# Optimization experiments

Measured on AMD Instinct MI355X. Metric: run time of the kernel, lower is better.

The kernel has to match this reference:

```python
import jax, jax.numpy as jnp
import numpy as np

D_MODEL = 1024
N_HEADS = 16
D_HEAD = D_MODEL // N_HEADS
FF = 4 * D_MODEL
B, S = 1, 2048
ROPE_BASE = 10000.0
LN_EPS = 1e-5


def setup_inputs() -> dict:
    key = jax.random.key(0)
    ks = jax.random.split(key, 12)
    sd = 0.02
    return {
        "x": jax.random.normal(ks[0], (B, S, D_MODEL), dtype=jnp.float32),
        # weights stored [in, out]
        "w_qkv": jax.random.normal(ks[1], (D_MODEL, 3 * D_MODEL), dtype=jnp.float32) * sd,
        "w_attn": jax.random.normal(ks[2], (D_MODEL, D_MODEL), dtype=jnp.float32) * sd,
        "b_attn": jnp.zeros((D_MODEL,), dtype=jnp.float32),
        "w_ff1": jax.random.normal(ks[3], (D_MODEL, FF), dtype=jnp.float32) * sd,
        "b_ff1": jnp.zeros((FF,), dtype=jnp.float32),
        "w_ff2": jax.random.normal(ks[4], (FF, D_MODEL), dtype=jnp.float32) * sd,
        "b_ff2": jnp.zeros((D_MODEL,), dtype=jnp.float32),
        "ln1_g": jnp.ones((D_MODEL,), dtype=jnp.float32),
        "ln1_b": jnp.zeros((D_MODEL,), dtype=jnp.float32),
        "ln2_g": jnp.ones((D_MODEL,), dtype=jnp.float32),
        "ln2_b": jnp.zeros((D_MODEL,), dtype=jnp.float32),
    }


def _layernorm(x, g, b):
    mu = jnp.mean(x, axis=-1, keepdims=True)
    var = jnp.mean(jnp.square(x - mu), axis=-1, keepdims=True)
    return (x - mu) * jax.lax.rsqrt(var + LN_EPS) * g + b


def _rope_cos_sin(seq_len, d_head, dtype):
    # scale=1.0 -> dynamic YaRN degenerates to vanilla RoPE with mscale=1
    inv_freq = 1.0 / (ROPE_BASE ** (jnp.arange(0, d_head, 2, dtype=jnp.float32) / d_head))
    pos = jnp.arange(seq_len, dtype=jnp.float32)
    freqs = pos[:, None] * inv_freq[None, :]          # [S, D/2]
    emb = jnp.concatenate([freqs, freqs], axis=-1)    # [S, D]
    return jnp.cos(emb).astype(dtype), jnp.sin(emb).astype(dtype)


def _rotate_half(x):
    x1, x2 = jnp.split(x, 2, axis=-1)
    return jnp.concatenate([-x2, x1], axis=-1)


def _apply_rope(q, k, cos, sin):
    # q,k: [B,S,H,D]; cos/sin: [S,D]
    c = cos[None, :, None, :]
    s = sin[None, :, None, :]
    return q * c + _rotate_half(q) * s, k * c + _rotate_half(k) * s


def _block(x, w_qkv, w_attn, b_attn, w_ff1, b_ff1, w_ff2, b_ff2,
           ln1_g, ln1_b, ln2_g, ln2_b):
    b, s, d = x.shape
    # --- attention sub-block (pre-norm) ---
    h = _layernorm(x, ln1_g, ln1_b)
    qkv = h @ w_qkv                                   # [B,S,3D]
    xq, xk, xv = jnp.split(qkv, 3, axis=-1)
    xq = xq.reshape(b, s, N_HEADS, D_HEAD)
    xk = xk.reshape(b, s, N_HEADS, D_HEAD)
    xv = xv.reshape(b, s, N_HEADS, D_HEAD)
    cos, sin = _rope_cos_sin(s, D_HEAD, x.dtype)
    xq, xk = _apply_rope(xq, xk, cos, sin)
    scale = 1.0 / np.sqrt(D_HEAD)
    scores = jnp.einsum("bqhd,bkhd->bhqk", xq, xk) * scale
    causal = jnp.tril(jnp.ones((s, s), dtype=bool))
    scores = jnp.where(causal[None, None], scores, jnp.finfo(scores.dtype).min)
    probs = jax.nn.softmax(scores, axis=-1)
    att = jnp.einsum("bhqk,bkhd->bqhd", probs, xv).reshape(b, s, d)
    x = x + (att @ w_attn + b_attn)
    # --- feed-forward sub-block (pre-norm) ---
    h2 = _layernorm(x, ln2_g, ln2_b)
    ff = jax.nn.gelu(h2 @ w_ff1 + b_ff1, approximate=False) @ w_ff2 + b_ff2
    return x + ff


def reference(x, w_qkv, w_attn, b_attn, w_ff1, b_ff1, w_ff2, b_ff2,
              ln1_g, ln1_b, ln2_g, ln2_b):
    return _block(x, w_qkv, w_attn, b_attn, w_ff1, b_ff1, w_ff2, b_ff2,
                  ln1_g, ln1_b, ln2_g, ln2_b)
```

## Files before the change

### kernel.cpp

```cpp
#include <hip/hip_runtime.h>
#include <hip/hip_bf16.h>
#include <stdint.h>

#define DM   1024
#define SEQ  2048
#define NH   16
#define DH   64
#define FFD  4096

typedef float  f32x4  __attribute__((ext_vector_type(4)));
typedef __bf16 bf16x8 __attribute__((ext_vector_type(8)));
typedef unsigned short u16;
typedef unsigned short u16x8 __attribute__((ext_vector_type(8)));

__device__ __forceinline__ u16 f2bf(float f){
    unsigned int u = __builtin_bit_cast(unsigned int, f);
    u = u + 0x7FFFu + ((u >> 16) & 1u);
    return (u16)(u >> 16);
}
__device__ __forceinline__ float bf2f(u16 v){
    unsigned int u = ((unsigned int)v) << 16;
    return __builtin_bit_cast(float, u);
}
__device__ __forceinline__ f32x4 zero4(){ f32x4 v; v[0]=0.f;v[1]=0.f;v[2]=0.f;v[3]=0.f; return v; }

__device__ __forceinline__ void gload_lds16(const void* g, void* l){
    __builtin_amdgcn_global_load_lds(
        (const __attribute__((address_space(1))) unsigned int*)(uintptr_t)g,
        (__attribute__((address_space(3))) unsigned int*)(uintptr_t)l,
        16, 0, 0);
}

__global__ __launch_bounds__(256) void transall_k(const float* __restrict__ s0, u16* __restrict__ d0,
                                                  const float* __restrict__ s1, u16* __restrict__ d1,
                                                  const float* __restrict__ s2, u16* __restrict__ d2,
                                                  const float* __restrict__ s3, u16* __restrict__ d3){
    __shared__ float tile[64][65];
    const int b = blockIdx.x;
    const float* src; u16* dst; int K, N, bx, by;
    if (b < 768)      { src = s0; dst = d0; K = 1024; N = 3072; bx = b % 48;          by = b / 48; }
    else if (b < 1024){ src = s1; dst = d1; K = 1024; N = 1024; bx = (b-768) % 16;    by = (b-768) / 16; }
    else if (b < 2048){ src = s2; dst = d2; K = 1024; N = 4096; bx = (b-1024) % 64;   by = (b-1024) / 64; }
    else              { src = s3; dst = d3; K = 4096; N = 1024; bx = (b-2048) % 16;   by = (b-2048) / 16; }
    const int n0 = bx * 64, k0 = by * 64;
    const int t = threadIdx.x;
#pragma unroll
    for (int i = 0; i < 16; ++i){
        int idx = t + i * 256;
        int r = idx >> 6, c = idx & 63;
        tile[r][c] = src[(size_t)(k0 + r) * N + n0 + c];
    }
    __syncthreads();
#pragma unroll
    for (int i = 0; i < 16; ++i){
        int idx = t + i * 256;
        int r = idx >> 6, c = idx & 63;
        dst[(size_t)(n0 + r) * K + k0 + c] = f2bf(tile[c][r]);
    }
}

__global__ __launch_bounds__(256) void ln_k(const float* __restrict__ in,
                                            const float* __restrict__ gw,
                                            const float* __restrict__ bw,
                                            u16* __restrict__ out){
    const int row = blockIdx.x, t = threadIdx.x;
    f32x4 vv = *((const f32x4*)(in + (size_t)row * DM) + t);
    float v[4];
#pragma unroll
    for (int j = 0; j < 4; ++j) v[j] = vv[j];
    float s = 0.f, ss = 0.f;
#pragma unroll
    for (int j = 0; j < 4; ++j){ s += v[j]; ss += v[j] * v[j]; }
#pragma unroll
    for (int off = 1; off < 64; off <<= 1){
        s  += __shfl_xor(s,  off, 64);
        ss += __shfl_xor(ss, off, 64);
    }
    __shared__ float rs_[4], rss_[4];
    const int w = t >> 6;
    if ((t & 63) == 0){ rs_[w] = s; rss_[w] = ss; }
    __syncthreads();
    s  = rs_[0] + rs_[1] + rs_[2] + rs_[3];
    ss = rss_[0] + rss_[1] + rss_[2] + rss_[3];
    const float mean = s * (1.f / DM);
    const float var  = ss * (1.f / DM) - mean * mean;
    const float rstd = rsqrtf(var + 1e-5f);
#pragma unroll
    for (int j = 0; j < 4; ++j){
        int c = t * 4 + j;
        out[(size_t)row * DM + c] = f2bf((v[j] - mean) * rstd * gw[c] + bw[c]);
    }
}

template<int TM, int TN, int WR, int WC, int EPI>
__global__ __launch_bounds__(256) void gemm_k(const u16* __restrict__ A,
                                              const u16* __restrict__ Bt,
                                              const float* __restrict__ bias,
                                              const float* __restrict__ resid,
                                              void* __restrict__ out,
                                              u16* __restrict__ qout,
                                              u16* __restrict__ kout,
                                              u16* __restrict__ vout,
                                              int M, int N, int K){
    constexpr int MR   = TM / WR / 16;
    constexpr int NR   = TN / WC / 16;
    constexpr int AISS = (TM * 64) / 4096;
    constexpr int BISS = (TN * 64) / 4096;
    __shared__ u16 ldsAll[2 * TM * 32 + 2 * TN * 32];
    u16* ldsA = ldsAll;
    u16* ldsB = ldsAll + 2 * TM * 32;
    const int t = threadIdx.x;
    const int L = t & 63, w = t >> 6;
    const int g = L >> 4, li = L & 15;
    const int wr = w / WC, wc = w % WC;
    const int rowbase = wr * (TM / WR);
    const int colbase = wc * (TN / WC);
    const int brow = blockIdx.x * TM, bcol = blockIdx.y * TN;

    const u16* aPtr = A  + (size_t)brow * K;
    const u16* bPtr = Bt + (size_t)bcol * K;

    f32x4 acc[MR][NR];
#pragma unroll
    for (int m = 0; m < MR; ++m)
#pragma unroll
        for (int n = 0; n < NR; ++n) acc[m][n] = zero4();

    auto STAGE = [&](int buf, int ko){
#pragma unroll
        for (int i = 0; i < AISS; ++i){
            int o = i * 256 + t;
            gload_lds16(aPtr + (size_t)(o >> 2) * K + (o & 3) * 8 + ko, &ldsA[buf * TM * 32 + o * 8]);
        }
#pragma unroll
        for (int i = 0; i < BISS; ++i){
            int o = i * 256 + t;
            gload_lds16(bPtr + (size_t)(o >> 2) * K + (o & 3) * 8 + ko, &ldsB[buf * TN * 32 + o * 8]);
        }
    };

    const int KT = K >> 5;
    int cur = 0;
    STAGE(0, 0);
    __syncthreads();
    for (int kt = 0; kt < KT; ++kt){
        if (kt + 1 < KT) STAGE(cur ^ 1, (kt + 1) * 32);
        bf16x8 af[MR], bfr[NR];
#pragma unroll
        for (int m = 0; m < MR; ++m)
            af[m]  = *(const bf16x8*)&ldsA[cur * TM * 32 + (rowbase + m * 16 + li) * 32 + g * 8];
#pragma unroll
        for (int n = 0; n < NR; ++n)
            bfr[n] = *(const bf16x8*)&ldsB[cur * TN * 32 + (colbase + n * 16 + li) * 32 + g * 8];
#pragma unroll
        for (int m = 0; m < MR; ++m)
#pragma unroll
            for (int n = 0; n < NR; ++n)
                acc[m][n] = __builtin_amdgcn_mfma_f32_16x16x32_bf16(af[m], bfr[n], acc[m][n], 0, 0, 0);
        __syncthreads();
        cur ^= 1;
    }

    if constexpr (EPI == 4){
        const int colabs = bcol + colbase;
        const int part = colabs >> 10;
        if (part < 2){
            u16* dst = (part == 0) ? qout : kout;
            const int h = (colabs >> 6) & 15;
            float freq[2];
#pragma unroll
            for (int n = 0; n < 2; ++n)
                freq[n] = powf(10000.f, -(float)(n * 16 + li) * (1.f / 32.f));
#pragma unroll
            for (int m = 0; m < MR; ++m)
#pragma unroll
                for (int r = 0; r < 4; ++r){
                    const int srow = brow + rowbase + m * 16 + g * 4 + r;
                    const size_t rb = ((size_t)h * SEQ + srow) * 64;
#pragma unroll
                    for (int n = 0; n < 2; ++n){
                        const int i = n * 16 + li;
                        float lo = acc[m][n][r], hi = acc[m][n + 2][r];
                        float sn, cs;
                        sincosf((float)srow * freq[n], &sn, &cs);
                        dst[rb + i]      = f2bf(lo * cs - hi * sn);
                        dst[rb + i + 32] = f2bf(hi * cs + lo * sn);
                    }
                }
        } else {
            u16* tileT = ldsAll;
            __syncthreads();
#pragma unroll
            for (int m = 0; m < MR; ++m)
#pragma unroll
                for (int n = 0; n < NR; ++n)
#pragma unroll
                    for (int r = 0; r < 4; ++r){
                        const int row = rowbase + m * 16 + g * 4 + r;
                        const int col = colbase + n * 16 + li;
                        tileT[col * 72 + row] = f2bf(acc[m][n][r]);
                    }
            __syncthreads();
            const int dv = t >> 1, half = t & 1;
            const int habs = ((bcol + dv) >> 6) & 15;
            const int dvl = dv & 63;
            u16* vrow = vout + ((size_t)habs * 64 + dvl) * SEQ + brow + half * 32;
#pragma unroll
            for (int j = 0; j < 4; ++j)
                *(u16x8*)(vrow + j * 8) = *(const u16x8*)&tileT[dv * 72 + half * 32 + j * 8];
        }
        return;
    }

#pragma unroll
    for (int m = 0; m < MR; ++m)
#pragma unroll
        for (int n = 0; n < NR; ++n)
#pragma unroll
            for (int r = 0; r < 4; ++r){
                const int row = brow + rowbase + m * 16 + g * 4 + r;
                const int col = bcol + colbase + n * 16 + li;
                float v = acc[m][n][r];
                if constexpr (EPI == 1){
                    v += bias[col] + resid[(size_t)row * N + col];
                    ((float*)out)[(size_t)row * N + col] = v;
                } else if constexpr (EPI == 2){
                    v += bias[col];
                    v = 0.5f * v * (1.f + erff(v * 0.70710678f));
                    ((u16*)out)[(size_t)row * N + col] = f2bf(v);
                } else {
                    v += bias[col] + resid[(size_t)row * N + col];
                    ((float*)out)[(size_t)row * N + col] = v;
                }
            }
}

#define LROW 72
#define NCHUNK 4
__global__ __launch_bounds__(256) void attn_k(const u16* __restrict__ Qh,
                                              const u16* __restrict__ Kh,
                                              const u16* __restrict__ VT,
                                              u16* __restrict__ Opart,
                                              float* __restrict__ ml){
    const int qb = blockIdx.x, h = blockIdx.y, c = blockIdx.z;
    const int qbase = qb * 64;
    const int kt0 = c * 8;
    const int ktEnd = min(kt0 + 8, qb + 1);
    if (kt0 >= qb + 1) return;

    __shared__ u16 ldsK[64 * LROW];
    __shared__ u16 ldsV[64 * LROW];
    __shared__ u16 ldsP[64 * LROW];
    const int t = threadIdx.x, L = t & 63, w = t >> 6, g = L >> 4, li = L & 15;

    bf16x8 aq[2];
    {
        const u16* qrow = Qh + ((size_t)h * SEQ + qbase + w * 16 + li) * 64;
        aq[0] = *(const bf16x8*)(qrow + g * 8);
        aq[1] = *(const bf16x8*)(qrow + 32 + g * 8);
    }
    f32x4 oacc[4];
#pragma unroll
    for (int n = 0; n < 4; ++n) oacc[n] = zero4();
    float mrow[4], lrow[4];
#pragma unroll
    for (int r = 0; r < 4; ++r){ mrow[r] = -3.0e4f; lrow[r] = 0.f; }

    for (int kt = kt0; kt < ktEnd; ++kt){
        const int kkbase = kt * 64;
        bf16x8 kreg[2], vreg[2];
        int rr_[2], ce_[2];
#pragma unroll
        for (int i = 0; i < 2; ++i){
            int o = i * 256 + t;
            rr_[i] = o >> 3; ce_[i] = (o & 7) * 8;
            kreg[i] = *(const bf16x8*)(Kh + ((size_t)h * SEQ + kkbase + rr_[i]) * 64 + ce_[i]);
            vreg[i] = *(const bf16x8*)(VT + ((size_t)h * 64 + rr_[i]) * SEQ + kkbase + ce_[i]);
        }
#pragma unroll
        for (int i = 0; i < 2; ++i){
            *(bf16x8*)(&ldsK[rr_[i] * LROW + ce_[i]]) = kreg[i];
            *(bf16x8*)(&ldsV[rr_[i] * LROW + ce_[i]]) = vreg[i];
        }
        __syncthreads();

        f32x4 sacc[4];
#pragma unroll
        for (int n = 0; n < 4; ++n) sacc[n] = zero4();
#pragma unroll
        for (int ds_ = 0; ds_ < 2; ++ds_){
#pragma unroll
            for (int n = 0; n < 4; ++n){
                const int kkl = n * 16 + li;
                bf16x8 bk = *(const bf16x8*)(&ldsK[kkl * LROW + ds_ * 32 + g * 8]);
                sacc[n] = __builtin_amdgcn_mfma_f32_16x16x32_bf16(aq[ds_], bk, sacc[n], 0, 0, 0);
            }
        }

        const bool diag = (kkbase == qbase);
        float pv[4][4], tmax[4];
#pragma unroll
        for (int r = 0; r < 4; ++r) tmax[r] = -3.0e4f;
#pragma unroll
        for (int n = 0; n < 4; ++n)
#pragma unroll
            for (int r = 0; r < 4; ++r){
                float sv = sacc[n][r] * 0.125f;
                if (diag){
                    int kkg = kkbase + n * 16 + li;
                    int qg  = qbase + w * 16 + g * 4 + r;
                    if (kkg > qg) sv = -3.0e4f;
                }
                pv[n][r] = sv;
                tmax[r] = fmaxf(tmax[r], sv);
            }
#pragma unroll
        for (int off = 1; off < 16; off <<= 1)
#pragma unroll
            for (int r = 0; r < 4; ++r) tmax[r] = fmaxf(tmax[r], __shfl_xor(tmax[r], off, 64));

        float alpha[4], psum[4];
#pragma unroll
        for (int r = 0; r < 4; ++r){
            float nm = fmaxf(mrow[r], tmax[r]);
            alpha[r] = __expf(mrow[r] - nm);
            mrow[r] = nm;
            psum[r] = 0.f;
        }
#pragma unroll
        for (int n = 0; n < 4; ++n)
#pragma unroll
            for (int r = 0; r < 4; ++r){
                float p = __expf(pv[n][r] - mrow[r]);
                pv[n][r] = p;
                psum[r] += p;
            }
#pragma unroll
        for (int off = 1; off < 16; off <<= 1)
#pragma unroll
            for (int r = 0; r < 4; ++r) psum[r] += __shfl_xor(psum[r], off, 64);
#pragma unroll
        for (int r = 0; r < 4; ++r){
            lrow[r] = lrow[r] * alpha[r] + psum[r];
#pragma unroll
            for (int n = 0; n < 4; ++n) oacc[n][r] *= alpha[r];
        }

#pragma unroll
        for (int n = 0; n < 4; ++n)
#pragma unroll
            for (int r = 0; r < 4; ++r){
                const int ql = w * 16 + g * 4 + r;
                const int kkl = n * 16 + li;
                ldsP[ql * LROW + kkl] = f2bf(pv[n][r]);
            }
        __syncthreads();

#pragma unroll
        for (int ks = 0; ks < 2; ++ks){
            const int qa = w * 16 + li;
            bf16x8 pa = *(const bf16x8*)(ldsP + qa * LROW + ks * 32 + g * 8);
#pragma unroll
            for (int n = 0; n < 4; ++n){
                const int dv = n * 16 + li;
                bf16x8 vb = *(const bf16x8*)(&ldsV[dv * LROW + ks * 32 + g * 8]);
                oacc[n] = __builtin_amdgcn_mfma_f32_16x16x32_bf16(pa, vb, oacc[n], 0, 0, 0);
            }
        }
        __syncthreads();
    }

    const size_t pb = (((size_t)(h * 32 + qb) * NCHUNK) + c) * 64;
#pragma unroll
    for (int n = 0; n < 4; ++n)
#pragma unroll
        for (int r = 0; r < 4; ++r){
            const int row = w * 16 + g * 4 + r;
            const int col = n * 16 + li;
            Opart[(pb + row) * 64 + col] = f2bf(oacc[n][r]);
        }
    if (li == 0){
#pragma unroll
        for (int r = 0; r < 4; ++r){
            const int row = w * 16 + g * 4 + r;
            ml[(pb + row) * 2]     = mrow[r];
            ml[(pb + row) * 2 + 1] = lrow[r];
        }
    }
}

__global__ __launch_bounds__(256) void combine_k(const u16* __restrict__ Opart,
                                                 const float* __restrict__ ml,
                                                 u16* __restrict__ att){
    const int qb = blockIdx.x, h = blockIdx.y;
    const int nact = ((qb * 64 + 63) >> 9) + 1;
    const int t = threadIdx.x;
    const int r = t >> 2, q4 = t & 3;
    const size_t pb = ((size_t)(h * 32 + qb) * NCHUNK) * 64;

    float mv[NCHUNK], lv[NCHUNK];
    float m = -3.0e30f;
    for (int c = 0; c < nact; ++c){
        mv[c] = ml[(pb + c * 64 + r) * 2];
        lv[c] = ml[(pb + c * 64 + r) * 2 + 1];
        m = fmaxf(m, mv[c]);
    }
    float wgt[NCHUNK], Lsum = 0.f;
    for (int c = 0; c < nact; ++c){
        wgt[c] = __expf(mv[c] - m);
        Lsum += wgt[c] * lv[c];
    }
    const float inv = 1.f / Lsum;

    float o[16];
#pragma unroll
    for (int j = 0; j < 16; ++j) o[j] = 0.f;
    for (int c = 0; c < nact; ++c){
        const u16* src = Opart + (pb + c * 64 + r) * 64 + q4 * 16;
        u16x8 a = *(const u16x8*)src;
        u16x8 b = *(const u16x8*)(src + 8);
#pragma unroll
        for (int e = 0; e < 8; ++e){
            o[e]     += wgt[c] * bf2f(a[e]);
            o[8 + e] += wgt[c] * bf2f(b[e]);
        }
    }
    const int qg = qb * 64 + r;
#pragma unroll
    for (int j = 0; j < 16; ++j){
        const int col = h * 64 + q4 * 16 + j;
        att[(size_t)qg * DM + col] = f2bf(o[j] * inv);
    }
}

extern "C" void kernel_launch(void* const* d_in, const int* in_sizes, int n_in,
                              void* d_out, int out_size, void* d_ws, size_t ws_size,
                              hipStream_t stream){
    (void)in_sizes; (void)n_in; (void)out_size; (void)ws_size;
    const float* x      = (const float*)d_in[0];
    const float* w_qkv  = (const float*)d_in[1];
    const float* w_attn = (const float*)d_in[2];
    const float* b_attn = (const float*)d_in[3];
    const float* w_ff1  = (const float*)d_in[4];
    const float* b_ff1  = (const float*)d_in[5];
    const float* w_ff2  = (const float*)d_in[6];
    const float* b_ff2  = (const float*)d_in[7];
    const float* ln1g   = (const float*)d_in[8];
    const float* ln1b   = (const float*)d_in[9];
    const float* ln2g   = (const float*)d_in[10];
    const float* ln2b   = (const float*)d_in[11];

    char* ws = (char*)d_ws;
    const size_t MB = 1u << 20;
    u16*   T1    = (u16*)(ws + 0);
    u16*   T2    = (u16*)(ws + 6  * MB);
    u16*   T3    = (u16*)(ws + 8  * MB);
    u16*   T4    = (u16*)(ws + 16 * MB);
    u16*   h1    = (u16*)(ws + 24 * MB);
    u16*   Qh    = (u16*)(ws + 28 * MB);
    u16*   Kh    = (u16*)(ws + 32 * MB);
    u16*   VT    = (u16*)(ws + 36 * MB);
    u16*   Opart = (u16*)(ws + 40 * MB);
    float* mlbuf = (float*)(ws + 56 * MB);
    u16*   att   = (u16*)(ws + 0);
    float* x2    = (float*)(ws + 40 * MB);
    u16*   h2    = (u16*)(ws + 4  * MB);
    u16*   ff    = (u16*)(ws + 24 * MB);

    transall_k<<<3072, 256, 0, stream>>>(w_qkv, T1, w_attn, T2, w_ff1, T3, w_ff2, T4);
    ln_k<<<SEQ, 256, 0, stream>>>(x, ln1g, ln1b, h1);
    gemm_k<64,128,2,2,4><<<dim3(32, 24), 256, 0, stream>>>(h1, T1, nullptr, nullptr, nullptr,
                                                           Qh, Kh, VT, SEQ, 3072, 1024);
    attn_k<<<dim3(32, 16, NCHUNK), 256, 0, stream>>>(Qh, Kh, VT, Opart, mlbuf);
    combine_k<<<dim3(32, 16), 256, 0, stream>>>(Opart, mlbuf, att);
    gemm_k<64,64,2,2,1><<<dim3(32, 16), 256, 0, stream>>>(att, T2, b_attn, x, x2,
                                                          nullptr, nullptr, nullptr, SEQ, 1024, 1024);
    ln_k<<<SEQ, 256, 0, stream>>>(x2, ln2g, ln2b, h2);
    gemm_k<64,128,1,4,2><<<dim3(32, 32), 256, 0, stream>>>(h2, T3, b_ff1, nullptr, ff,
                                                           nullptr, nullptr, nullptr, SEQ, 4096, 1024);
    gemm_k<64,64,2,2,3><<<dim3(32, 16), 256, 0, stream>>>(ff, T4, b_ff2, x2, (float*)d_out,
                                                          nullptr, nullptr, nullptr, SEQ, 1024, 4096);
}
```

Before: 207.2 us.

## Rewrite attention as per-wave 32x32 MFMA flash kernel without LDS

The attention kernel now gives each wavefront its own 32-query tile and 8-key-tile chunk, ordered longest-first. It uses 32x32x16 bf16 MFMA with S computed transposed, so softmax rows sit in registers and P is packed with v_cvt_pk_bf16 and cross-half shuffles instead of going through LDS. K tiles are prefetched into registers one iteration ahead, and all __syncthreads are gone, which removes LDS staging and barrier costs. The combine kernel and the partial-buffer indexing change to a compact triangular job layout, with twice as many combine blocks. The trade-off is that K and V are read straight from global memory with no sharing across waves, which raises global and L2 traffic.

```diff
diff --git a/kernel.cpp b/kernel.cpp
--- a/kernel.cpp
+++ b/kernel.cpp
@@ -9,8 +9,10 @@
 #define FFD  4096
 
 typedef float  f32x4  __attribute__((ext_vector_type(4)));
+typedef float  f32x16 __attribute__((ext_vector_type(16)));
 typedef __bf16 bf16x8 __attribute__((ext_vector_type(8)));
 typedef unsigned short u16;
+typedef unsigned short u16x4v __attribute__((ext_vector_type(4)));
 typedef unsigned short u16x8 __attribute__((ext_vector_type(8)));
 
 __device__ __forceinline__ u16 f2bf(float f){
@@ -23,6 +25,11 @@
     return __builtin_bit_cast(float, u);
 }
 __device__ __forceinline__ f32x4 zero4(){ f32x4 v; v[0]=0.f;v[1]=0.f;v[2]=0.f;v[3]=0.f; return v; }
+__device__ __forceinline__ unsigned int cvtpk(float lo, float hi){
+    unsigned int r;
+    asm("v_cvt_pk_bf16_f32 %0, %1, %2" : "=v"(r) : "v"(lo), "v"(hi));
+    return r;
+}
 
 __device__ __forceinline__ void gload_lds16(const void* g, void* l){
     __builtin_amdgcn_global_load_lds(
@@ -235,202 +242,177 @@
             }
 }
 
-#define LROW 72
-#define NCHUNK 4
+#define CHT 8
 __global__ __launch_bounds__(256) void attn_k(const u16* __restrict__ Qh,
                                               const u16* __restrict__ Kh,
                                               const u16* __restrict__ VT,
                                               u16* __restrict__ Opart,
                                               float* __restrict__ ml){
-    const int qb = blockIdx.x, h = blockIdx.y, c = blockIdx.z;
-    const int qbase = qb * 64;
-    const int kt0 = c * 8;
-    const int ktEnd = min(kt0 + 8, qb + 1);
-    if (kt0 >= qb + 1) return;
-
-    __shared__ u16 ldsK[64 * LROW];
-    __shared__ u16 ldsV[64 * LROW];
-    __shared__ u16 ldsP[64 * LROW];
-    const int t = threadIdx.x, L = t & 63, w = t >> 6, g = L >> 4, li = L & 15;
-
-    bf16x8 aq[2];
-    {
-        const u16* qrow = Qh + ((size_t)h * SEQ + qbase + w * 16 + li) * 64;
-        aq[0] = *(const bf16x8*)(qrow + g * 8);
-        aq[1] = *(const bf16x8*)(qrow + 32 + g * 8);
-    }
-    f32x4 oacc[4];
-#pragma unroll
-    for (int n = 0; n < 4; ++n) oacc[n] = zero4();
-    float mrow[4], lrow[4];
-#pragma unroll
-    for (int r = 0; r < 4; ++r){ mrow[r] = -3.0e4f; lrow[r] = 0.f; }
-
-    for (int kt = kt0; kt < ktEnd; ++kt){
-        const int kkbase = kt * 64;
-        bf16x8 kreg[2], vreg[2];
-        int rr_[2], ce_[2];
-#pragma unroll
-        for (int i = 0; i < 2; ++i){
-            int o = i * 256 + t;
-            rr_[i] = o >> 3; ce_[i] = (o & 7) * 8;
-            kreg[i] = *(const bf16x8*)(Kh + ((size_t)h * SEQ + kkbase + rr_[i]) * 64 + ce_[i]);
-            vreg[i] = *(const bf16x8*)(VT + ((size_t)h * 64 + rr_[i]) * SEQ + kkbase + ce_[i]);
-        }
-#pragma unroll
-        for (int i = 0; i < 2; ++i){
-            *(bf16x8*)(&ldsK[rr_[i] * LROW + ce_[i]]) = kreg[i];
-            *(bf16x8*)(&ldsV[rr_[i] * LROW + ce_[i]]) = vreg[i];
-        }
-        __syncthreads();
-
-        f32x4 sacc[4];
-#pragma unroll
-        for (int n = 0; n < 4; ++n) sacc[n] = zero4();
-#pragma unroll
-        for (int ds_ = 0; ds_ < 2; ++ds_){
-#pragma unroll
-            for (int n = 0; n < 4; ++n){
-                const int kkl = n * 16 + li;
-                bf16x8 bk = *(const bf16x8*)(&ldsK[kkl * LROW + ds_ * 32 + g * 8]);
-                sacc[n] = __builtin_amdgcn_mfma_f32_16x16x32_bf16(aq[ds_], bk, sacc[n], 0, 0, 0);
+    const int t = threadIdx.x, w = t >> 6, L = t & 63;
+    const int job = blockIdx.x * 4 + w;
+    const int h   = job >> 9;
+    const int rem = job & 511;
+    const int qt  = 63 - (rem & 63);
+    const int c   = rem >> 6;
+    if (c * CHT > qt) return;
+    const int t0 = c * CHT;
+    const int tEnd = min(t0 + CHT, qt + 1);
+    const int l31 = L & 31, H = L >> 5;
+    const int qbase = qt * 32;
+
+    const u16* kB = Kh + (size_t)h * SEQ * 64;
+    const u16* vB = VT + (size_t)h * 64 * SEQ;
+
+    const u16* qrow = Qh + ((size_t)h * SEQ + qbase + l31) * 64 + H * 8;
+    bf16x8 qf0 = *(const bf16x8*)(qrow);
+    bf16x8 qf1 = *(const bf16x8*)(qrow + 16);
+    bf16x8 qf2 = *(const bf16x8*)(qrow + 32);
+    bf16x8 qf3 = *(const bf16x8*)(qrow + 48);
+
+    const u16* krow0 = kB + (size_t)(t0 * 32 + l31) * 64 + H * 8;
+    bf16x8 kc0 = *(const bf16x8*)(krow0);
+    bf16x8 kc1 = *(const bf16x8*)(krow0 + 16);
+    bf16x8 kc2 = *(const bf16x8*)(krow0 + 32);
+    bf16x8 kc3 = *(const bf16x8*)(krow0 + 48);
+
+    f32x16 O0, O1;
+#pragma unroll
+    for (int i = 0; i < 16; ++i){ O0[i] = 0.f; O1[i] = 0.f; }
+    float m = -3.0e4f, lsum = 0.f;
+
+    for (int tt = t0; tt < tEnd; ++tt){
+        const u16* va0 = vB + (size_t)l31 * SEQ + tt * 32 + H * 8;
+        const u16* va1 = va0 + (size_t)32 * SEQ;
+        bf16x8 v00 = *(const bf16x8*)(va0);
+        bf16x8 v01 = *(const bf16x8*)(va0 + 16);
+        bf16x8 v10 = *(const bf16x8*)(va1);
+        bf16x8 v11 = *(const bf16x8*)(va1 + 16);
+
+        f32x16 st;
+#pragma unroll
+        for (int i = 0; i < 16; ++i) st[i] = 0.f;
+        st = __builtin_amdgcn_mfma_f32_32x32x16_bf16(kc0, qf0, st, 0, 0, 0);
+        st = __builtin_amdgcn_mfma_f32_32x32x16_bf16(kc1, qf1, st, 0, 0, 0);
+        st = __builtin_amdgcn_mfma_f32_32x32x16_bf16(kc2, qf2, st, 0, 0, 0);
+        st = __builtin_amdgcn_mfma_f32_32x32x16_bf16(kc3, qf3, st, 0, 0, 0);
+
+        const bool more = (tt + 1 < tEnd);
+        bf16x8 kn0, kn1, kn2, kn3;
+        if (more){
+            const u16* krow = kB + (size_t)((tt + 1) * 32 + l31) * 64 + H * 8;
+            kn0 = *(const bf16x8*)(krow);
+            kn1 = *(const bf16x8*)(krow + 16);
+            kn2 = *(const bf16x8*)(krow + 32);
+            kn3 = *(const bf16x8*)(krow + 48);
+        }
+
+        const bool diag = (tt == qt);
+        float sv[16];
+#pragma unroll
+        for (int i = 0; i < 16; ++i){
+            float x = st[i] * 0.125f;
+            if (diag){
+                int kkl = (i & 3) + 8 * (i >> 2) + 4 * H;
+                if (kkl > l31) x = -3.0e4f;
             }
-        }
-
-        const bool diag = (kkbase == qbase);
-        float pv[4][4], tmax[4];
-#pragma unroll
-        for (int r = 0; r < 4; ++r) tmax[r] = -3.0e4f;
-#pragma unroll
-        for (int n = 0; n < 4; ++n)
-#pragma unroll
-            for (int r = 0; r < 4; ++r){
-                float sv = sacc[n][r] * 0.125f;
-                if (diag){
-                    int kkg = kkbase + n * 16 + li;
-                    int qg  = qbase + w * 16 + g * 4 + r;
-                    if (kkg > qg) sv = -3.0e4f;
-                }
-                pv[n][r] = sv;
-                tmax[r] = fmaxf(tmax[r], sv);
-            }
-#pragma unroll
-        for (int off = 1; off < 16; off <<= 1)
-#pragma unroll
-            for (int r = 0; r < 4; ++r) tmax[r] = fmaxf(tmax[r], __shfl_xor(tmax[r], off, 64));
-
-        float alpha[4], psum[4];
-#pragma unroll
-        for (int r = 0; r < 4; ++r){
-            float nm = fmaxf(mrow[r], tmax[r]);
-            alpha[r] = __expf(mrow[r] - nm);
-            mrow[r] = nm;
-            psum[r] = 0.f;
-        }
-#pragma unroll
-        for (int n = 0; n < 4; ++n)
-#pragma unroll
-            for (int r = 0; r < 4; ++r){
-                float p = __expf(pv[n][r] - mrow[r]);
-                pv[n][r] = p;
-                psum[r] += p;
-            }
-#pragma unroll
-        for (int off = 1; off < 16; off <<= 1)
-#pragma unroll
-            for (int r = 0; r < 4; ++r) psum[r] += __shfl_xor(psum[r], off, 64);
-#pragma unroll
-        for (int r = 0; r < 4; ++r){
-            lrow[r] = lrow[r] * alpha[r] + psum[r];
-#pragma unroll
-            for (int n = 0; n < 4; ++n) oacc[n][r] *= alpha[r];
-        }
-
-#pragma unroll
-        for (int n = 0; n < 4; ++n)
-#pragma unroll
-            for (int r = 0; r < 4; ++r){
-                const int ql = w * 16 + g * 4 + r;
-                const int kkl = n * 16 + li;
-                ldsP[ql * LROW + kkl] = f2bf(pv[n][r]);
-            }
-        __syncthreads();
-
-#pragma unroll
-        for (int ks = 0; ks < 2; ++ks){
-            const int qa = w * 16 + li;
-            bf16x8 pa = *(const bf16x8*)(ldsP + qa * LROW + ks * 32 + g * 8);
-#pragma unroll
-            for (int n = 0; n < 4; ++n){
-                const int dv = n * 16 + li;
-                bf16x8 vb = *(const bf16x8*)(&ldsV[dv * LROW + ks * 32 + g * 8]);
-                oacc[n] = __builtin_amdgcn_mfma_f32_16x16x32_bf16(pa, vb, oacc[n], 0, 0, 0);
-            }
-        }
-        __syncthreads();
-    }
-
-    const size_t pb = (((size_t)(h * 32 + qb) * NCHUNK) + c) * 64;
-#pragma unroll
-    for (int n = 0; n < 4; ++n)
-#pragma unroll
-        for (int r = 0; r < 4; ++r){
-            const int row = w * 16 + g * 4 + r;
-            const int col = n * 16 + li;
-            Opart[(pb + row) * 64 + col] = f2bf(oacc[n][r]);
-        }
-    if (li == 0){
-#pragma unroll
-        for (int r = 0; r < 4; ++r){
-            const int row = w * 16 + g * 4 + r;
-            ml[(pb + row) * 2]     = mrow[r];
-            ml[(pb + row) * 2 + 1] = lrow[r];
-        }
+            sv[i] = x;
+        }
+        float smax = sv[0];
+#pragma unroll
+        for (int i = 1; i < 16; ++i) smax = fmaxf(smax, sv[i]);
+        smax = fmaxf(smax, __shfl_xor(smax, 32, 64));
+        const float nm = fmaxf(m, smax);
+        const float alpha = __expf(m - nm);
+        m = nm;
+        float ps = 0.f;
+#pragma unroll
+        for (int i = 0; i < 16; ++i){ sv[i] = __expf(sv[i] - m); ps += sv[i]; }
+        ps += __shfl_xor(ps, 32, 64);
+        lsum = lsum * alpha + ps;
+#pragma unroll
+        for (int i = 0; i < 16; ++i){ O0[i] *= alpha; O1[i] *= alpha; }
+
+        unsigned int A0 = cvtpk(sv[0],  sv[1]),  A1 = cvtpk(sv[2],  sv[3]);
+        unsigned int B0 = cvtpk(sv[4],  sv[5]),  B1 = cvtpk(sv[6],  sv[7]);
+        unsigned int C0 = cvtpk(sv[8],  sv[9]),  C1 = cvtpk(sv[10], sv[11]);
+        unsigned int D0 = cvtpk(sv[12], sv[13]), D1 = cvtpk(sv[14], sv[15]);
+        unsigned int eA0 = (unsigned int)__shfl_xor((int)A0, 32, 64);
+        unsigned int eA1 = (unsigned int)__shfl_xor((int)A1, 32, 64);
+        unsigned int eB0 = (unsigned int)__shfl_xor((int)B0, 32, 64);
+        unsigned int eB1 = (unsigned int)__shfl_xor((int)B1, 32, 64);
+        unsigned int eC0 = (unsigned int)__shfl_xor((int)C0, 32, 64);
+        unsigned int eC1 = (unsigned int)__shfl_xor((int)C1, 32, 64);
+        unsigned int eD0 = (unsigned int)__shfl_xor((int)D0, 32, 64);
+        unsigned int eD1 = (unsigned int)__shfl_xor((int)D1, 32, 64);
+        union Uw { unsigned int w[4]; bf16x8 v; };
+        Uw f0, f1;
+        f0.w[0] = H ? eB0 : A0;  f0.w[1] = H ? eB1 : A1;
+        f0.w[2] = H ? B0  : eA0; f0.w[3] = H ? B1  : eA1;
+        f1.w[0] = H ? eD0 : C0;  f1.w[1] = H ? eD1 : C1;
+        f1.w[2] = H ? D0  : eC0; f1.w[3] = H ? D1  : eC1;
+
+        O0 = __builtin_amdgcn_mfma_f32_32x32x16_bf16(v00, f0.v, O0, 0, 0, 0);
+        O0 = __builtin_amdgcn_mfma_f32_32x32x16_bf16(v01, f1.v, O0, 0, 0, 0);
+        O1 = __builtin_amdgcn_mfma_f32_32x32x16_bf16(v10, f0.v, O1, 0, 0, 0);
+        O1 = __builtin_amdgcn_mfma_f32_32x32x16_bf16(v11, f1.v, O1, 0, 0, 0);
+
+        if (more){ kc0 = kn0; kc1 = kn1; kc2 = kn2; kc3 = kn3; }
+    }
+
+    const int mq = qt >> 3, rq = qt & 7;
+    const int jobd = h * 288 + (qt + 4 * mq * (mq - 1) + rq * mq) + c;
+    const size_t ob = (size_t)jobd * (32 * 64);
+    const int q = l31;
+#pragma unroll
+    for (int f = 0; f < 2; ++f){
+        const int dv0 = f * 32;
+#pragma unroll
+        for (int k = 0; k < 4; ++k){
+            u16x4v pkv;
+#pragma unroll
+            for (int e = 0; e < 4; ++e)
+                pkv[e] = f2bf(f == 0 ? O0[k * 4 + e] : O1[k * 4 + e]);
+            *(u16x4v*)(Opart + ob + (size_t)q * 64 + dv0 + 8 * k + 4 * H) = pkv;
+        }
+    }
+    if (H == 0){
+        ml[((size_t)jobd * 32 + q) * 2]     = m;
+        ml[((size_t)jobd * 32 + q) * 2 + 1] = lsum;
     }
 }
 
 __global__ __launch_bounds__(256) void combine_k(const u16* __restrict__ Opart,
                                                  const float* __restrict__ ml,
                                                  u16* __restrict__ att){
-    const int qb = blockIdx.x, h = blockIdx.y;
-    const int nact = ((qb * 64 + 63) >> 9) + 1;
+    const int qt = blockIdx.x, h = blockIdx.y;
+    const int nact = (qt >> 3) + 1;
+    const int mq = qt >> 3, rq = qt & 7;
+    const int j0 = h * 288 + (qt + 4 * mq * (mq - 1) + rq * mq);
     const int t = threadIdx.x;
-    const int r = t >> 2, q4 = t & 3;
-    const size_t pb = ((size_t)(h * 32 + qb) * NCHUNK) * 64;
-
-    float mv[NCHUNK], lv[NCHUNK];
+    const int q = t >> 3, dv0 = (t & 7) * 8;
+
     float m = -3.0e30f;
-    for (int c = 0; c < nact; ++c){
-        mv[c] = ml[(pb + c * 64 + r) * 2];
-        lv[c] = ml[(pb + c * 64 + r) * 2 + 1];
-        m = fmaxf(m, mv[c]);
-    }
-    float wgt[NCHUNK], Lsum = 0.f;
-    for (int c = 0; c < nact; ++c){
-        wgt[c] = __expf(mv[c] - m);
-        Lsum += wgt[c] * lv[c];
-    }
-    const float inv = 1.f / Lsum;
-
-    float o[16];
-#pragma unroll
-    for (int j = 0; j < 16; ++j) o[j] = 0.f;
-    for (int c = 0; c < nact; ++c){
-        const u16* src = Opart + (pb + c * 64 + r) * 64 + q4 * 16;
+    for (int cc = 0; cc < nact; ++cc)
+        m = fmaxf(m, ml[((size_t)(j0 + cc) * 32 + q) * 2]);
+    float Ls = 0.f;
+    float o[8];
+#pragma unroll
+    for (int j = 0; j < 8; ++j) o[j] = 0.f;
+    for (int cc = 0; cc < nact; ++cc){
+        const float mv = ml[((size_t)(j0 + cc) * 32 + q) * 2];
+        const float lv = ml[((size_t)(j0 + cc) * 32 + q) * 2 + 1];
+        const float wgt = __expf(mv - m);
+        Ls += wgt * lv;
+        const u16* src = Opart + ((size_t)(j0 + cc) * 32 + q) * 64 + dv0;
         u16x8 a = *(const u16x8*)src;
-        u16x8 b = *(const u16x8*)(src + 8);
-#pragma unroll
-        for (int e = 0; e < 8; ++e){
-            o[e]     += wgt[c] * bf2f(a[e]);
-            o[8 + e] += wgt[c] * bf2f(b[e]);
-        }
-    }
-    const int qg = qb * 64 + r;
-#pragma unroll
-    for (int j = 0; j < 16; ++j){
-        const int col = h * 64 + q4 * 16 + j;
-        att[(size_t)qg * DM + col] = f2bf(o[j] * inv);
-    }
+#pragma unroll
+        for (int e = 0; e < 8; ++e) o[e] += wgt * bf2f(a[e]);
+    }
+    const float inv = 1.f / Ls;
+    const int qg = qt * 32 + q;
+#pragma unroll
+    for (int j = 0; j < 8; ++j)
+        att[(size_t)qg * DM + h * 64 + dv0 + j] = f2bf(o[j] * inv);
 }
 
 extern "C" void kernel_launch(void* const* d_in, const int* in_sizes, int n_in,
@@ -461,7 +443,7 @@
     u16*   Kh    = (u16*)(ws + 32 * MB);
     u16*   VT    = (u16*)(ws + 36 * MB);
     u16*   Opart = (u16*)(ws + 40 * MB);
-    float* mlbuf = (float*)(ws + 56 * MB);
+    float* mlbuf = (float*)(ws + 59 * MB);
     u16*   att   = (u16*)(ws + 0);
     float* x2    = (float*)(ws + 40 * MB);
     u16*   h2    = (u16*)(ws + 4  * MB);
@@ -471,8 +453,8 @@
     ln_k<<<SEQ, 256, 0, stream>>>(x, ln1g, ln1b, h1);
     gemm_k<64,128,2,2,4><<<dim3(32, 24), 256, 0, stream>>>(h1, T1, nullptr, nullptr, nullptr,
                                                            Qh, Kh, VT, SEQ, 3072, 1024);
-    attn_k<<<dim3(32, 16, NCHUNK), 256, 0, stream>>>(Qh, Kh, VT, Opart, mlbuf);
-    combine_k<<<dim3(32, 16), 256, 0, stream>>>(Opart, mlbuf, att);
+    attn_k<<<2048, 256, 0, stream>>>(Qh, Kh, VT, Opart, mlbuf);
+    combine_k<<<dim3(64, 16), 256, 0, stream>>>(Opart, mlbuf, att);
     gemm_k<64,64,2,2,1><<<dim3(32, 16), 256, 0, stream>>>(att, T2, b_attn, x, x2,
                                                           nullptr, nullptr, nullptr, SEQ, 1024, 1024);
     ln_k<<<SEQ, 256, 0, stream>>>(x2, ln2g, ln2b, h2);
```

New measurement: 218.9 us. 5.7% more time.
